# Kernel tuning notes

Hardware: AMD Instinct MI355X
Metric: run time of the kernel (lower is better)

## Reference

```python
import jax, jax.numpy as jnp
import numpy as np
import math

B, S, H = 2, 2048, 3072
N_HEADS, N_KV_HEADS, HEAD_DIM = 32, 8, 96
ROPE_THETA = 10000.0
OP_SIZE = N_HEADS * HEAD_DIM + 2 * N_KV_HEADS * HEAD_DIM  # 4608


def setup_inputs() -> dict:
    key = jax.random.key(0)
    k1, k2, k3 = jax.random.split(key, 3)
    hidden_states = jax.random.normal(k1, (B, S, H), dtype=jnp.float32)
    # additive causal mask: 0 on/below diagonal, -inf-ish above
    neg = jnp.finfo(jnp.float32).min
    causal = jnp.where(jnp.tril(jnp.ones((S, S), dtype=bool)), 0.0, neg)
    attention_mask = jnp.broadcast_to(causal[None, None], (B, 1, S, S)).astype(jnp.float32)
    # torch nn.Linear convention: weight [out_features, in_features]
    w_qkv = jax.random.normal(k2, (OP_SIZE, H), dtype=jnp.float32) * 0.02
    w_o = jax.random.normal(k3, (H, H), dtype=jnp.float32) * 0.02
    position_ids = jnp.broadcast_to(jnp.arange(S, dtype=jnp.int32)[None], (B, S))
    return {"hidden_states": hidden_states, "attention_mask": attention_mask,
            "w_qkv": w_qkv, "w_o": w_o, "position_ids": position_ids}


def _rotate_half(x):
    half = x.shape[-1] // 2
    return jnp.concatenate([-x[..., half:], x[..., :half]], axis=-1)


def _rope_cos_sin(position_ids, head_dim, theta):
    # Phi3RotaryEmbedding (no scaling)
    inv_freq = 1.0 / (theta ** (jnp.arange(0, head_dim, 2, dtype=jnp.float32) / head_dim))
    freqs = position_ids.astype(jnp.float32)[:, :, None] * inv_freq[None, None, :]  # [b,s,d/2]
    emb = jnp.concatenate([freqs, freqs], axis=-1)  # [b,s,d]
    return jnp.cos(emb), jnp.sin(emb)


def reference(hidden_states, attention_mask, w_qkv, w_o, position_ids):
    b, s, _ = hidden_states.shape
    qkv = jnp.einsum('bsh,oh->bso', hidden_states, w_qkv)  # quantized qkv_proj (fp emulation)
    q_pos = N_HEADS * HEAD_DIM
    kv_pos = q_pos + N_KV_HEADS * HEAD_DIM
    q = qkv[..., :q_pos].reshape(b, s, N_HEADS, HEAD_DIM).transpose(0, 2, 1, 3)
    k = qkv[..., q_pos:kv_pos].reshape(b, s, N_KV_HEADS, HEAD_DIM).transpose(0, 2, 1, 3)
    v = qkv[..., kv_pos:].reshape(b, s, N_KV_HEADS, HEAD_DIM).transpose(0, 2, 1, 3)

    cos, sin = _rope_cos_sin(position_ids, HEAD_DIM, ROPE_THETA)
    cos, sin = cos[:, None], sin[:, None]  # [b,1,s,d]
    q = q * cos + _rotate_half(q) * sin
    k = k * cos + _rotate_half(k) * sin

    # repeat_kv: GQA expand kv heads to query heads
    groups = N_HEADS // N_KV_HEADS
    k = jnp.repeat(k, groups, axis=1)  # [b,h,s,d]
    v = jnp.repeat(v, groups, axis=1)

    # quantized QK^T matmul (fp emulation)
    scores = jnp.einsum('bhqd,bhkd->bhqk', q, k) / math.sqrt(HEAD_DIM)
    scores = scores + attention_mask  # additive causal mask
    attn = jax.nn.softmax(scores.astype(jnp.float32), axis=-1).astype(v.dtype)
    # dropout p=0 (eval); quantized attn @ V matmul (fp emulation)
    out = jnp.einsum('bhqk,bhkd->bhqd', attn, v)
    out = out.transpose(0, 2, 1, 3).reshape(b, s, N_HEADS * HEAD_DIM)
    out = jnp.einsum('bso,ho->bsh', out, w_o)  # quantized o_proj
    return out
```

## Files before the change

### kernel.cpp

```cpp
#include <hip/hip_runtime.h>
#include <hip/hip_bf16.h>
#include <math.h>

#define S_LEN 2048
#define HDIM  3072
#define NH    32
#define NKV   8
#define HD    96
#define OPSZ  4608
#define QPOS  3072
#define KPOS  3840

typedef short  short8 __attribute__((ext_vector_type(8)));
typedef short  short4v __attribute__((ext_vector_type(4)));
typedef float  f32x4  __attribute__((ext_vector_type(4)));
typedef unsigned short us4 __attribute__((ext_vector_type(4)));

typedef __attribute__((address_space(1))) const unsigned int* gas1_t;
typedef __attribute__((address_space(3))) unsigned int* las3_t;

__device__ __forceinline__ void gl_lds16(const void* g, void* l) {
  __builtin_amdgcn_global_load_lds((gas1_t)g, (las3_t)l, 16, 0, 0);
}

#define VMCNT(n) asm volatile("s_waitcnt vmcnt(" #n ")" ::: "memory")

__device__ __forceinline__ unsigned short f2b(float f) {
  union { float f; unsigned u; } x; x.f = f;
  unsigned r = x.u + 0x7fffu + ((x.u >> 16) & 1u);
  return (unsigned short)(r >> 16);
}
__device__ __forceinline__ float b2f(unsigned short b) {
  union { unsigned u; float f; } x; x.u = ((unsigned)b) << 16;
  return x.f;
}

__device__ __forceinline__ short4v pack_bf16_4(float p0, float p1, float p2, float p3) {
  unsigned u0 = __builtin_bit_cast(unsigned, p0) + 0x8000u;
  unsigned u1 = __builtin_bit_cast(unsigned, p1) + 0x8000u;
  unsigned u2 = __builtin_bit_cast(unsigned, p2) + 0x8000u;
  unsigned u3 = __builtin_bit_cast(unsigned, p3) + 0x8000u;
  unsigned lo = __builtin_amdgcn_perm(u1, u0, 0x07060302u);
  unsigned hi = __builtin_amdgcn_perm(u3, u2, 0x07060302u);
  uint2 q; q.x = lo; q.y = hi;
  return __builtin_bit_cast(short4v, q);
}

__global__ __launch_bounds__(256) void k_convert(const float* __restrict__ src,
                                                 unsigned short* __restrict__ dst, int n4) {
  int i = blockIdx.x * 256 + threadIdx.x;
  if (i >= n4) return;
  float4 v = ((const float4*)src)[i];
  us4 o;
  o[0] = f2b(v.x); o[1] = f2b(v.y); o[2] = f2b(v.z); o[3] = f2b(v.w);
  ((us4*)dst)[i] = o;
}

#define GSLOT 14336
template<int OUTBF>
__global__ __launch_bounds__(512, 2) void k_gemm_pipe(const unsigned short* __restrict__ A,
                                                      const unsigned short* __restrict__ Bt,
                                                      void* __restrict__ Cout,
                                                      int M, int N, int K, int GX) {
  __shared__ unsigned short lds[4 * GSLOT];

  const int NC = K >> 5;
  const int tid = threadIdx.x;
  const int lane = tid & 63;
  const int wave = tid >> 6;
  const int wm = wave >> 2, wn = wave & 3;
  const int lr = lane & 15, lg = lane >> 4;
  const int prh = lr >> 1, bit = lr & 1;

  const int nwg = gridDim.x;
  const int id  = blockIdx.x;
  const int sw  = (id & 7) * (nwg >> 3) + (id >> 3);
  const int bx  = sw % GX, by = sw / GX;
  const int m0 = by * 256, n0 = bx * 192;

  const int i0 = tid, i1 = 512 + tid;
  const int p0 = i0 >> 3, gl0 = (i0 & 7) ^ (p0 & 7);
  const int p1 = i1 >> 3, gl1 = (i1 & 7) ^ (p1 & 7);
  const unsigned short* aG0 = A + (size_t)(m0 + 2 * p0 + (gl0 >> 2)) * K + (gl0 & 3) * 8;
  const unsigned short* aG1 = A + (size_t)(m0 + 2 * p1 + (gl1 >> 2)) * K + (gl1 & 3) * 8;
  const int aO0 = i0 * 8, aO1 = i1 * 8;
  const int q0 = i0 >> 3, hl0 = (i0 & 7) ^ (q0 & 7);
  const int q1 = i1 >> 3, hl1 = (i1 & 7) ^ (q1 & 7);
  const unsigned short* bG0 = Bt + (size_t)(n0 + 2 * q0 + (hl0 >> 2)) * K + (hl0 & 3) * 8;
  const unsigned short* bG1 = Bt + (size_t)(n0 + 2 * q1 + (hl1 >> 2)) * K + (hl1 & 3) * 8;
  const int bO0 = 8192 + i0 * 8, bO1 = 8192 + i1 * 8;
  const bool loB2 = (tid < 256);

  auto stageA = [&](int c) {
    unsigned short* sb = &lds[(c & 3) * GSLOT];
    gl_lds16(aG0 + c * 32, sb + aO0);
    gl_lds16(aG1 + c * 32, sb + aO1);
  };
  auto stageB = [&](int c) {
    unsigned short* sb = &lds[(c & 3) * GSLOT];
    gl_lds16(bG0 + c * 32, sb + bO0);
    if (loB2) gl_lds16(bG1 + c * 32, sb + bO1);
  };

  const int gp  = ((bit << 2) + lg) ^ prh;
  const int aRd = wm * 4096 + prh * 64 + gp * 8;
  const int bRd = 8192 + wn * 1536 + prh * 64 + gp * 8;

  f32x4 acc[8][3];
#pragma unroll
  for (int mf = 0; mf < 8; mf++)
#pragma unroll
    for (int nf = 0; nf < 3; nf++)
#pragma unroll
      for (int r = 0; r < 4; r++) acc[mf][nf][r] = 0.0f;

  stageA(0); stageB(0);
  stageA(1); stageB(1);
  stageA(2); stageB(2);
  if (wave < 4) { VMCNT(8); } else { VMCNT(6); }
  __builtin_amdgcn_s_barrier();
  __builtin_amdgcn_sched_barrier(0);

  for (int c = 0; c < NC; ++c) {
    const unsigned short* sb = &lds[(c & 3) * GSLOT];
    short8 af[4], bf[3];
#pragma unroll
    for (int mf = 0; mf < 4; mf++) af[mf] = *(const short8*)&sb[aRd + mf * 512];
#pragma unroll
    for (int nf = 0; nf < 3; nf++) bf[nf] = *(const short8*)&sb[bRd + nf * 512];
    if (c + 3 < NC) stageA(c + 3);
    __builtin_amdgcn_s_barrier();
    __builtin_amdgcn_s_setprio(1);
#pragma unroll
    for (int mf = 0; mf < 4; mf++)
#pragma unroll
      for (int nf = 0; nf < 3; nf++)
        acc[mf][nf] = __builtin_amdgcn_mfma_f32_16x16x32_bf16(af[mf], bf[nf], acc[mf][nf], 0, 0, 0);
    __builtin_amdgcn_s_setprio(0);
    __builtin_amdgcn_s_barrier();
#pragma unroll
    for (int mf = 0; mf < 4; mf++) af[mf] = *(const short8*)&sb[aRd + (4 + mf) * 512];
    if (c + 3 < NC) stageB(c + 3);
    __builtin_amdgcn_s_barrier();
    __builtin_amdgcn_s_setprio(1);
#pragma unroll
    for (int mf = 0; mf < 4; mf++)
#pragma unroll
      for (int nf = 0; nf < 3; nf++)
        acc[4 + mf][nf] = __builtin_amdgcn_mfma_f32_16x16x32_bf16(af[mf], bf[nf], acc[4 + mf][nf], 0, 0, 0);
    __builtin_amdgcn_s_setprio(0);
    if (c < NC - 3)        { if (wave < 4) { VMCNT(8); } else { VMCNT(6); } }
    else if (c == NC - 3)  { if (wave < 4) { VMCNT(4); } else { VMCNT(3); } }
    else if (c == NC - 2)  { VMCNT(0); }
    if (c + 1 < NC) {
      __builtin_amdgcn_s_barrier();
      __builtin_amdgcn_sched_barrier(0);
    }
  }

#pragma unroll
  for (int mf = 0; mf < 8; mf++)
#pragma unroll
    for (int nf = 0; nf < 3; nf++)
#pragma unroll
      for (int r = 0; r < 4; r++) {
        int row = m0 + wm * 128 + mf * 16 + lg * 4 + r;
        int col = n0 + wn * 48 + nf * 16 + lr;
        if (OUTBF) ((unsigned short*)Cout)[(size_t)row * N + col] = f2b(acc[mf][nf][r]);
        else       ((float*)Cout)[(size_t)row * N + col] = acc[mf][nf][r];
      }
}

__global__ __launch_bounds__(256) void k_rope(const unsigned short* __restrict__ qkv,
                                              const int* __restrict__ pos_ids,
                                              unsigned short* __restrict__ Qb,
                                              unsigned short* __restrict__ Kb) {
  __shared__ float cs[96], sn[96];
  int blk = blockIdx.x;
  int b = blk >> 11, s = blk & 2047;
  int t = threadIdx.x;
  int pos = pos_ids[blk];
  if (t < 48) {
    double e = -((double)(2 * t) / 96.0) * log(10000.0);
    float invf = (float)exp(e);
    float a = (float)pos * invf;
    float c, si;
    sincosf(a, &si, &c);
    cs[t] = c; cs[t + 48] = c;
    sn[t] = si; sn[t + 48] = si;
  }
  __syncthreads();
  const unsigned short* row = qkv + (size_t)blk * OPSZ;
  const float qscale = 0.1020620726159658f;
  for (int o = t; o < KPOS; o += 256) {
    int d = o % 96;
    float x  = b2f(row[o]);
    float xp = b2f(row[d < 48 ? o + 48 : o - 48]);
    float rot = (d < 48) ? -xp : xp;
    float val = x * cs[d] + rot * sn[d];
    if (o < QPOS) {
      int h = o / 96;
      Qb[((size_t)(b * NH + h) * S_LEN + s) * HD + d] = f2b(val * qscale);
    } else {
      int kh = (o - QPOS) / 96;
      Kb[((size_t)(b * NKV + kh) * S_LEN + s) * HD + d] = f2b(val);
    }
  }
}

__global__ __launch_bounds__(256) void k_vtrans(const unsigned short* __restrict__ qkv,
                                                unsigned short* __restrict__ Vt) {
  int blk = blockIdx.x;
  int st = blk & 31, kh = (blk >> 5) & 7, b = blk >> 8;
  int s0 = st * 64;
  __shared__ unsigned short tile[96][65];
  int t = threadIdx.x;
#pragma unroll
  for (int c = 0; c < 24; c++) {
    int idx = c * 256 + t;
    int ls = idx / 96, d = idx % 96;
    tile[d][ls] = qkv[(size_t)(b * S_LEN + s0 + ls) * OPSZ + KPOS + kh * 96 + d];
  }
  __syncthreads();
#pragma unroll
  for (int c = 0; c < 24; c++) {
    int idx = c * 256 + t;
    int d = idx >> 6, ls = idx & 63;
    Vt[((size_t)(b * NKV + kh) * HD + d) * S_LEN + s0 + ls] = tile[d][ls];
  }
}

__global__ __launch_bounds__(512, 4) void k_flash(const unsigned short* __restrict__ Qb,
                                                  const unsigned short* __restrict__ Kb,
                                                  const unsigned short* __restrict__ Vt,
                                                  unsigned short* __restrict__ attn) {
  __shared__ unsigned short smem[24832];
  __shared__ float Lsh[128 * 8];
  unsigned short* Ks  = smem;
  unsigned short* Vs  = smem + 6144;
  unsigned short* QPs = smem + 12288;
  float* Osh = (float*)smem;

  int blk = blockIdx.x;
  int j = blk & 7;
  int h = (blk >> 3) & 31;
  int b = blk >> 8;
  int kh = h >> 2;
  int tid = threadIdx.x, lane = tid & 63, wave = tid >> 6;
  int lr = lane & 15, lg = lane >> 4;
  int qg = wave >> 1, kg = wave & 1;
  const int swz = (lr >> 1) & 3;

  const unsigned short* ksrc = Kb + (size_t)(b * NKV + kh) * S_LEN * HD;
  const unsigned short* vsrc = Vt + (size_t)(b * NKV + kh) * HD * S_LEN;

  for (int half = 0; half < 2; half++) {
    int qtile = half ? (15 - j) : j;
    int q0 = qtile * 128;
    const unsigned short* qsrc = Qb + ((size_t)(b * NH + h) * S_LEN + q0) * HD;

    __syncthreads();
#pragma unroll
    for (int p = 0; p < 3; p++) {
      int gi = p * 512 + tid;
      int pl = gi >> 9, wp = gi & 511;
      int r = wp >> 2, s = wp & 3;
      int l = pl * 4 + (s ^ ((r >> 1) & 3));
      gl_lds16(qsrc + (size_t)r * HD + l * 8, &QPs[gi * 8]);
    }
#pragma unroll
    for (int p = 0; p < 3; p++) {
      int gi = p * 512 + tid;
      if (gi < 768) {
        int pl = gi >> 8, wp = gi & 255;
        int r = wp >> 2, s = wp & 3;
        int l = pl * 4 + (s ^ ((r >> 1) & 3));
        gl_lds16(ksrc + (size_t)r * HD + l * 8, &Ks[gi * 8]);
      } else {
        int gi2 = gi - 768;
        int pl = (gi2 >= 384) ? 1 : 0;
        int rem = gi2 - pl * 384;
        int d = rem >> 2, s = rem & 3;
        int l = s ^ ((d >> 1) & 3);
        gl_lds16(vsrc + (size_t)d * S_LEN + pl * 32 + l * 8, &Vs[gi2 * 8]);
      }
    }
    __syncthreads();

    short8 qf[2][3];
#pragma unroll
    for (int qt = 0; qt < 2; qt++)
#pragma unroll
      for (int ds = 0; ds < 3; ds++)
        qf[qt][ds] = *(const short8*)&QPs[ds * 4096 + (qg * 32 + qt * 16 + lr) * 32 + (lg ^ swz) * 8];

    f32x4 oacc[2][6];
#pragma unroll
    for (int qt = 0; qt < 2; qt++)
#pragma unroll
      for (int dt = 0; dt < 6; dt++)
#pragma unroll
        for (int r = 0; r < 4; r++) oacc[qt][dt][r] = 0.0f;
    float lsum[2] = {0.0f, 0.0f};

    int nk = qtile * 2 + 2;
    for (int it = 0; it < nk; it++) {
      int k0 = it * 64;
      f32x4 sc[2][2];
#pragma unroll
      for (int kt = 0; kt < 2; kt++)
#pragma unroll
        for (int qt = 0; qt < 2; qt++)
#pragma unroll
          for (int r = 0; r < 4; r++) sc[kt][qt][r] = 0.0f;
#pragma unroll
      for (int kt = 0; kt < 2; kt++)
#pragma unroll
        for (int ds = 0; ds < 3; ds++) {
          short8 kf = *(const short8*)&Ks[ds * 2048 + (kg * 32 + kt * 16 + lr) * 32 + (lg ^ swz) * 8];
#pragma unroll
          for (int qt = 0; qt < 2; qt++)
            sc[kt][qt] = __builtin_amdgcn_mfma_f32_16x16x32_bf16(kf, qf[qt][ds], sc[kt][qt], 0, 0, 0);
        }
      if (it >= nk - 2) {
#pragma unroll
        for (int kt = 0; kt < 2; kt++)
#pragma unroll
          for (int qt = 0; qt < 2; qt++) {
            int qrow = q0 + qg * 32 + qt * 16 + lr;
            int keyb = k0 + kg * 32 + kt * 16 + lg * 4;
#pragma unroll
            for (int r = 0; r < 4; r++)
              if (keyb + r > qrow) sc[kt][qt][r] = -3.0e38f;
          }
      }
      short4v pf[2][2];
#pragma unroll
      for (int kt = 0; kt < 2; kt++)
#pragma unroll
        for (int qt = 0; qt < 2; qt++) {
          float p0 = __expf(sc[kt][qt][0]);
          float p1 = __expf(sc[kt][qt][1]);
          float p2 = __expf(sc[kt][qt][2]);
          float p3 = __expf(sc[kt][qt][3]);
          lsum[qt] += (p0 + p1) + (p2 + p3);
          pf[kt][qt] = pack_bf16_4(p0, p1, p2, p3);
        }
#pragma unroll
      for (int kt = 0; kt < 2; kt++)
#pragma unroll
        for (int dt = 0; dt < 6; dt++) {
          short4v vf = *(const short4v*)&Vs[kg * 3072 + (dt * 16 + lr) * 32 +
                                           (((kt * 2 + (lg >> 1)) ^ swz) * 8) + (lg & 1) * 4];
#pragma unroll
          for (int qt = 0; qt < 2; qt++)
            oacc[qt][dt] = __builtin_amdgcn_mfma_f32_16x16x16bf16_1k(pf[kt][qt], vf, oacc[qt][dt], 0, 0, 0);
        }
      __syncthreads();
      if (it + 1 < nk) {
        int k0n = (it + 1) * 64;
#pragma unroll
        for (int p = 0; p < 3; p++) {
          int gi = p * 512 + tid;
          if (gi < 768) {
            int pl = gi >> 8, wp = gi & 255;
            int r = wp >> 2, s = wp & 3;
            int l = pl * 4 + (s ^ ((r >> 1) & 3));
            gl_lds16(ksrc + (size_t)(k0n + r) * HD + l * 8, &Ks[gi * 8]);
          } else {
            int gi2 = gi - 768;
            int pl = (gi2 >= 384) ? 1 : 0;
            int rem = gi2 - pl * 384;
            int d = rem >> 2, s = rem & 3;
            int l = s ^ ((d >> 1) & 3);
            gl_lds16(vsrc + (size_t)d * S_LEN + k0n + pl * 32 + l * 8, &Vs[gi2 * 8]);
          }
        }
        __syncthreads();
      }
    }
    if (kg == 0) {
#pragma unroll
      for (int qt = 0; qt < 2; qt++)
#pragma unroll
        for (int dt = 0; dt < 6; dt++)
#pragma unroll
          for (int r = 0; r < 4; r++)
            Osh[(qg * 32 + qt * 16 + lg * 4 + r) * 97 + dt * 16 + lr] = oacc[qt][dt][r];
    }
#pragma unroll
    for (int qt = 0; qt < 2; qt++)
      Lsh[(qg * 32 + qt * 16 + lr) * 8 + kg * 4 + lg] = lsum[qt];
    __syncthreads();
    if (kg == 1) {
      float linv[2][4];
#pragma unroll
      for (int qt = 0; qt < 2; qt++)
#pragma unroll
        for (int r = 0; r < 4; r++) {
          int row = qg * 32 + qt * 16 + lg * 4 + r;
          float4 a = *(const float4*)&Lsh[row * 8];
          float4 c = *(const float4*)&Lsh[row * 8 + 4];
          linv[qt][r] = 1.0f / ((a.x + a.y + a.z + a.w) + (c.x + c.y + c.z + c.w));
        }
#pragma unroll
      for (int qt = 0; qt < 2; qt++)
#pragma unroll
        for (int dt = 0; dt < 6; dt++)
#pragma unroll
          for (int r = 0; r < 4; r++) {
            int rowl = qg * 32 + qt * 16 + lg * 4 + r;
            float v = Osh[rowl * 97 + dt * 16 + lr] + oacc[qt][dt][r];
            int row = q0 + rowl;
            int col = h * 96 + dt * 16 + lr;
            attn[(size_t)(b * S_LEN + row) * HDIM + col] = f2b(v * linv[qt][r]);
          }
    }
  }
}

extern "C" void kernel_launch(void* const* d_in, const int* in_sizes, int n_in,
                              void* d_out, int out_size, void* d_ws, size_t ws_size,
                              hipStream_t stream) {
  const float* hidden = (const float*)d_in[0];
  const float* w_qkv  = (const float*)d_in[2];
  const float* w_o    = (const float*)d_in[3];
  const int*   posids = (const int*)d_in[4];

  const size_t M = 4096;
  unsigned short* hidden_bf = (unsigned short*)d_ws;
  unsigned short* wqkv_bf   = hidden_bf + M * HDIM;
  unsigned short* wo_bf     = wqkv_bf + (size_t)OPSZ * HDIM;
  unsigned short* qkv_bf    = wo_bf + (size_t)HDIM * HDIM;
  unsigned short* Qb   = hidden_bf;
  unsigned short* Kb   = wqkv_bf;
  unsigned short* Vt   = wqkv_bf + (size_t)NKV * 2 * S_LEN * HD;
  unsigned short* attn = qkv_bf;

  int n4h = (int)(M * HDIM / 4);
  int n4q = (int)((size_t)OPSZ * HDIM / 4);
  int n4o = (int)((size_t)HDIM * HDIM / 4);
  k_convert<<<(n4h + 255) / 256, 256, 0, stream>>>(hidden, hidden_bf, n4h);
  k_convert<<<(n4q + 255) / 256, 256, 0, stream>>>(w_qkv, wqkv_bf, n4q);
  k_convert<<<(n4o + 255) / 256, 256, 0, stream>>>(w_o, wo_bf, n4o);

  k_gemm_pipe<1><<<384, 512, 0, stream>>>(hidden_bf, wqkv_bf, qkv_bf,
                                          (int)M, OPSZ, HDIM, OPSZ / 192);
  k_rope<<<(int)M, 256, 0, stream>>>(qkv_bf, posids, Qb, Kb);
  k_vtrans<<<2 * NKV * (S_LEN / 64), 256, 0, stream>>>(qkv_bf, Vt);
  k_flash<<<2 * NH * 8, 512, 0, stream>>>(Qb, Kb, Vt, attn);
  k_gemm_pipe<0><<<256, 512, 0, stream>>>(attn, wo_bf, d_out,
                                          (int)M, HDIM, HDIM, HDIM / 192);
}
```

Before: 545.8 us.

## Templatize GEMM N-tile, use 256x288 tiles for QKV projection and 4x2 wave grid

The pipelined GEMM is now templated on the number of N fragments, and the wave layout changes from 2x4 to 4x2 (each wave covers 64 rows and BN/2 columns). The QKV projection uses a 256x288 tile with 256 workgroups, where it previously used 256x192 with 384, so the grid is a single even wave over the CUs and tail imbalance is reduced. It also loads B fragments in two halves rather than A halves, which changes the per-chunk LDS reads and the vmcnt accounting. Separately, the RoPE frequency and sin/cos computation moves from double-precision exp/log to fast float intrinsics, which may cost some accuracy at large positions.

After: 499.0 us. 1.09x faster.

```diff
diff --git a/kernel.cpp b/kernel.cpp
--- a/kernel.cpp
+++ b/kernel.cpp
@@ -56,19 +56,23 @@
   ((us4*)dst)[i] = o;
 }
 
-#define GSLOT 14336
-template<int OUTBF>
+template<int OUTBF, int NF>
 __global__ __launch_bounds__(512, 2) void k_gemm_pipe(const unsigned short* __restrict__ A,
                                                       const unsigned short* __restrict__ Bt,
                                                       void* __restrict__ Cout,
                                                       int M, int N, int K, int GX) {
+  constexpr int BN    = NF * 32;
+  constexpr int GSLOT = 8192 + BN * 32;
+  constexpr int BGR   = BN * 4;
+  constexpr int NFA   = (NF + 1) / 2;
+  constexpr int NFB   = NF - NFA;
   __shared__ unsigned short lds[4 * GSLOT];
 
   const int NC = K >> 5;
   const int tid = threadIdx.x;
   const int lane = tid & 63;
   const int wave = tid >> 6;
-  const int wm = wave >> 2, wn = wave & 3;
+  const int wm = wave & 3, wn = wave >> 2;
   const int lr = lane & 15, lg = lane >> 4;
   const int prh = lr >> 1, bit = lr & 1;
 
@@ -76,20 +80,25 @@
   const int id  = blockIdx.x;
   const int sw  = (id & 7) * (nwg >> 3) + (id >> 3);
   const int bx  = sw % GX, by = sw / GX;
-  const int m0 = by * 256, n0 = bx * 192;
+  const int m0 = by * 256, n0 = bx * BN;
 
   const int i0 = tid, i1 = 512 + tid;
-  const int p0 = i0 >> 3, gl0 = (i0 & 7) ^ (p0 & 7);
-  const int p1 = i1 >> 3, gl1 = (i1 & 7) ^ (p1 & 7);
-  const unsigned short* aG0 = A + (size_t)(m0 + 2 * p0 + (gl0 >> 2)) * K + (gl0 & 3) * 8;
-  const unsigned short* aG1 = A + (size_t)(m0 + 2 * p1 + (gl1 >> 2)) * K + (gl1 & 3) * 8;
+  const int p0 = i0 >> 3, g0 = (i0 & 7) ^ (p0 & 7);
+  const int p1 = i1 >> 3, g1 = (i1 & 7) ^ (p1 & 7);
+  const unsigned short* aG0 = A + (size_t)(m0 + 2 * p0 + (g0 >> 2)) * K + (g0 & 3) * 8;
+  const unsigned short* aG1 = A + (size_t)(m0 + 2 * p1 + (g1 >> 2)) * K + (g1 & 3) * 8;
   const int aO0 = i0 * 8, aO1 = i1 * 8;
-  const int q0 = i0 >> 3, hl0 = (i0 & 7) ^ (q0 & 7);
-  const int q1 = i1 >> 3, hl1 = (i1 & 7) ^ (q1 & 7);
-  const unsigned short* bG0 = Bt + (size_t)(n0 + 2 * q0 + (hl0 >> 2)) * K + (hl0 & 3) * 8;
-  const unsigned short* bG1 = Bt + (size_t)(n0 + 2 * q1 + (hl1 >> 2)) * K + (hl1 & 3) * 8;
+
+  const int q0 = i0 >> 3, h0 = (i0 & 7) ^ (q0 & 7);
+  const int q1 = i1 >> 3, h1 = (i1 & 7) ^ (q1 & 7);
+  const unsigned short* bG0 = Bt + (size_t)(n0 + 2 * q0 + (h0 >> 2)) * K + (h0 & 3) * 8;
+  const unsigned short* bG1 = Bt + (size_t)(n0 + 2 * q1 + (h1 >> 2)) * K + (h1 & 3) * 8;
   const int bO0 = 8192 + i0 * 8, bO1 = 8192 + i1 * 8;
-  const bool loB2 = (tid < 256);
+  const int i2 = 1024 + (tid & 127);
+  const int q2 = i2 >> 3, h2 = (i2 & 7) ^ (q2 & 7);
+  const unsigned short* bG2 = Bt + (size_t)(n0 + ((2 * q2 + (h2 >> 2)) < BN ? (2 * q2 + (h2 >> 2)) : 0)) * K + (h2 & 3) * 8;
+  const int bO2 = 8192 + i2 * 8;
+  const bool xb = (NF == 9) ? (tid < 128) : (tid < 256);
 
   auto stageA = [&](int c) {
     unsigned short* sb = &lds[(c & 3) * GSLOT];
@@ -99,59 +108,71 @@
   auto stageB = [&](int c) {
     unsigned short* sb = &lds[(c & 3) * GSLOT];
     gl_lds16(bG0 + c * 32, sb + bO0);
-    if (loB2) gl_lds16(bG1 + c * 32, sb + bO1);
+    if constexpr (NF == 9) {
+      gl_lds16(bG1 + c * 32, sb + bO1);
+      if (xb) gl_lds16(bG2 + c * 32, sb + bO2);
+    } else {
+      if (xb) gl_lds16(bG1 + c * 32, sb + bO1);
+    }
   };
 
   const int gp  = ((bit << 2) + lg) ^ prh;
-  const int aRd = wm * 4096 + prh * 64 + gp * 8;
-  const int bRd = 8192 + wn * 1536 + prh * 64 + gp * 8;
-
-  f32x4 acc[8][3];
-#pragma unroll
-  for (int mf = 0; mf < 8; mf++)
-#pragma unroll
-    for (int nf = 0; nf < 3; nf++)
+  const int aRd = wm * 2048 + prh * 64 + gp * 8;
+  const int bRd = 8192 + wn * (BN * 16) + prh * 64 + gp * 8;
+
+  f32x4 acc[4][NF];
+#pragma unroll
+  for (int mf = 0; mf < 4; mf++)
+#pragma unroll
+    for (int nf = 0; nf < NF; nf++)
 #pragma unroll
       for (int r = 0; r < 4; r++) acc[mf][nf][r] = 0.0f;
+
+#define VM_STEADY() do { \
+    if constexpr (NF == 9) { if (wave < 2) { VMCNT(10); } else { VMCNT(8); } } \
+    else                   { if (wave < 4) { VMCNT(8);  } else { VMCNT(6); } } } while (0)
+#define VM_TAIL1() do { \
+    if constexpr (NF == 9) { if (wave < 2) { VMCNT(5); } else { VMCNT(4); } } \
+    else                   { if (wave < 4) { VMCNT(4); } else { VMCNT(3); } } } while (0)
 
   stageA(0); stageB(0);
   stageA(1); stageB(1);
   stageA(2); stageB(2);
-  if (wave < 4) { VMCNT(8); } else { VMCNT(6); }
+  VM_STEADY();
   __builtin_amdgcn_s_barrier();
   __builtin_amdgcn_sched_barrier(0);
 
   for (int c = 0; c < NC; ++c) {
     const unsigned short* sb = &lds[(c & 3) * GSLOT];
-    short8 af[4], bf[3];
+    short8 af[4], bA[NFA], bB[NFB];
 #pragma unroll
     for (int mf = 0; mf < 4; mf++) af[mf] = *(const short8*)&sb[aRd + mf * 512];
 #pragma unroll
-    for (int nf = 0; nf < 3; nf++) bf[nf] = *(const short8*)&sb[bRd + nf * 512];
+    for (int nf = 0; nf < NFA; nf++) bA[nf] = *(const short8*)&sb[bRd + nf * 512];
     if (c + 3 < NC) stageA(c + 3);
     __builtin_amdgcn_s_barrier();
     __builtin_amdgcn_s_setprio(1);
 #pragma unroll
     for (int mf = 0; mf < 4; mf++)
 #pragma unroll
-      for (int nf = 0; nf < 3; nf++)
-        acc[mf][nf] = __builtin_amdgcn_mfma_f32_16x16x32_bf16(af[mf], bf[nf], acc[mf][nf], 0, 0, 0);
+      for (int nf = 0; nf < NFA; nf++)
+        acc[mf][nf] = __builtin_amdgcn_mfma_f32_16x16x32_bf16(af[mf], bA[nf], acc[mf][nf], 0, 0, 0);
     __builtin_amdgcn_s_setprio(0);
     __builtin_amdgcn_s_barrier();
 #pragma unroll
-    for (int mf = 0; mf < 4; mf++) af[mf] = *(const short8*)&sb[aRd + (4 + mf) * 512];
+    for (int nf = 0; nf < NFB; nf++) bB[nf] = *(const short8*)&sb[bRd + (NFA + nf) * 512];
     if (c + 3 < NC) stageB(c + 3);
     __builtin_amdgcn_s_barrier();
     __builtin_amdgcn_s_setprio(1);
 #pragma unroll
     for (int mf = 0; mf < 4; mf++)
 #pragma unroll
-      for (int nf = 0; nf < 3; nf++)
-        acc[4 + mf][nf] = __builtin_amdgcn_mfma_f32_16x16x32_bf16(af[mf], bf[nf], acc[4 + mf][nf], 0, 0, 0);
+      for (int nf = 0; nf < NFB; nf++)
+        acc[mf][NFA + nf] = __builtin_amdgcn_mfma_f32_16x16x32_bf16(af[mf], bB[nf], acc[mf][NFA + nf], 0, 0, 0);
     __builtin_amdgcn_s_setprio(0);
-    if (c < NC - 3)        { if (wave < 4) { VMCNT(8); } else { VMCNT(6); } }
-    else if (c == NC - 3)  { if (wave < 4) { VMCNT(4); } else { VMCNT(3); } }
-    else if (c == NC - 2)  { VMCNT(0); }
+    if (c < NC - 3)       { VM_STEADY(); }
+    else if (c == NC - 3) { VM_TAIL1(); }
+    else if (c == NC - 2) { VMCNT(0); }
     if (c + 1 < NC) {
       __builtin_amdgcn_s_barrier();
       __builtin_amdgcn_sched_barrier(0);
@@ -159,16 +180,18 @@
   }
 
 #pragma unroll
-  for (int mf = 0; mf < 8; mf++)
-#pragma unroll
-    for (int nf = 0; nf < 3; nf++)
+  for (int mf = 0; mf < 4; mf++)
+#pragma unroll
+    for (int nf = 0; nf < NF; nf++)
 #pragma unroll
       for (int r = 0; r < 4; r++) {
-        int row = m0 + wm * 128 + mf * 16 + lg * 4 + r;
-        int col = n0 + wn * 48 + nf * 16 + lr;
+        int row = m0 + wm * 64 + mf * 16 + lg * 4 + r;
+        int col = n0 + wn * (BN / 2) + nf * 16 + lr;
         if (OUTBF) ((unsigned short*)Cout)[(size_t)row * N + col] = f2b(acc[mf][nf][r]);
         else       ((float*)Cout)[(size_t)row * N + col] = acc[mf][nf][r];
       }
+#undef VM_STEADY
+#undef VM_TAIL1
 }
 
 __global__ __launch_bounds__(256) void k_rope(const unsigned short* __restrict__ qkv,
@@ -181,11 +204,11 @@
   int t = threadIdx.x;
   int pos = pos_ids[blk];
   if (t < 48) {
-    double e = -((double)(2 * t) / 96.0) * log(10000.0);
-    float invf = (float)exp(e);
+    float e = -((float)(2 * t) / 96.0f) * 9.210340371976184f;
+    float invf = __expf(e);
     float a = (float)pos * invf;
     float c, si;
-    sincosf(a, &si, &c);
+    __sincosf(a, &si, &c);
     cs[t] = c; cs[t + 48] = c;
     sn[t] = si; sn[t + 48] = si;
   }
@@ -444,11 +467,11 @@
   k_convert<<<(n4q + 255) / 256, 256, 0, stream>>>(w_qkv, wqkv_bf, n4q);
   k_convert<<<(n4o + 255) / 256, 256, 0, stream>>>(w_o, wo_bf, n4o);
 
-  k_gemm_pipe<1><<<384, 512, 0, stream>>>(hidden_bf, wqkv_bf, qkv_bf,
-                                          (int)M, OPSZ, HDIM, OPSZ / 192);
+  k_gemm_pipe<1, 9><<<256, 512, 0, stream>>>(hidden_bf, wqkv_bf, qkv_bf,
+                                             (int)M, OPSZ, HDIM, OPSZ / 288);
   k_rope<<<(int)M, 256, 0, stream>>>(qkv_bf, posids, Qb, Kb);
   k_vtrans<<<2 * NKV * (S_LEN / 64), 256, 0, stream>>>(qkv_bf, Vt);
   k_flash<<<2 * NH * 8, 512, 0, stream>>>(Qb, Kb, Vt, attn);
-  k_gemm_pipe<0><<<256, 512, 0, stream>>>(attn, wo_bf, d_out,
-                                          (int)M, HDIM, HDIM, HDIM / 192);
-}
+  k_gemm_pipe<0, 6><<<256, 512, 0, stream>>>(attn, wo_bf, d_out,
+                                             (int)M, HDIM, HDIM, HDIM / 192);
+}
```
